# Kernel tuning notes

Hardware: AMD Instinct MI355X
Metric: run time of the kernel (lower is better)

The kernel has to match this reference:

```python
import jax, jax.numpy as jnp
import numpy as np

D_MODEL = 1024
N_HEADS = 16
HEAD_DIM = D_MODEL // N_HEADS


def setup_inputs() -> dict:
    key = jax.random.key(0)
    ks = jax.random.split(key, 5)
    B, S = 2, 2048
    x = jax.random.normal(ks[0], (B, S, D_MODEL), dtype=jnp.float32)
    # nn.Linear weights: [out_features, in_features]
    s_in = 1.0 / np.sqrt(D_MODEL)
    qkv_w = jax.random.uniform(ks[1], (3 * D_MODEL, D_MODEL), jnp.float32, -s_in, s_in)
    qkv_b = jax.random.uniform(ks[2], (3 * D_MODEL,), jnp.float32, -s_in, s_in)
    out_w = jax.random.uniform(ks[3], (D_MODEL, D_MODEL), jnp.float32, -s_in, s_in)
    out_b = jax.random.uniform(ks[4], (D_MODEL,), jnp.float32, -s_in, s_in)
    return {"x": x, "qkv_w": qkv_w, "qkv_b": qkv_b, "out_w": out_w, "out_b": out_b}


def reference(x, qkv_w, qkv_b, out_w, out_b):
    B, S, D = x.shape
    H, Hd = N_HEADS, HEAD_DIM
    scale = 1.0 / np.sqrt(Hd)
    qkv = jnp.einsum('bsd,ed->bse', x, qkv_w) + qkv_b  # [B,S,3D]
    qkv = qkv.reshape(B, S, 3, H, Hd)
    q = qkv[:, :, 0].transpose(0, 2, 1, 3)  # [B,H,S,Hd]
    k = qkv[:, :, 1].transpose(0, 2, 1, 3)
    v = qkv[:, :, 2].transpose(0, 2, 1, 3)
    scores = jnp.einsum('bhqd,bhkd->bhqk', q, k) * scale  # [B,H,S,S]
    causal = jnp.triu(jnp.ones((S, S), dtype=bool), k=1)
    scores = jnp.where(causal[None, None], -jnp.inf, scores)
    probs = jax.nn.softmax(scores, axis=-1)
    out = jnp.einsum('bhqk,bhkd->bhqd', probs, v)  # [B,H,S,Hd]
    out = out.transpose(0, 2, 1, 3).reshape(B, S, D)
    out = jnp.einsum('bsd,ed->bse', out, out_w) + out_b
    return out
```

## Files before the change

kernel.cpp:

```cpp
#include <hip/hip_runtime.h>
#include <hip/hip_bf16.h>

#define SEQ    2048
#define DMODEL 1024
#define NHEAD  16
#define HDIM   64
#define BATCH  2
#define NTOK   (BATCH * SEQ)

#define N_X   (NTOK * DMODEL)
#define N_WQ  (3 * DMODEL * DMODEL)
#define N_BQ  (3 * DMODEL)
#define N_WO  (DMODEL * DMODEL)
#define N_BO  (DMODEL)
#define N_CANON (N_X + N_WQ + N_BQ + N_WO + N_BO)

#define NEG_SENT (-1.0e30f)
#define QSCALE 0.1803368801111f

typedef __attribute__((ext_vector_type(8))) short short8;
typedef __attribute__((ext_vector_type(4))) short short4v;
typedef __attribute__((ext_vector_type(4))) float f32x4;

#define MFMA_BF16(A, B, C) __builtin_amdgcn_mfma_f32_16x16x32_bf16((A), (B), (C), 0, 0, 0)

static __device__ __forceinline__ short8 load8(const __hip_bfloat16* p) {
    return *(const short8*)p;
}

static __device__ __forceinline__ void async16(const void* g, void* l) {
    __builtin_amdgcn_global_load_lds(
        (const __attribute__((address_space(1))) unsigned int*)g,
        (__attribute__((address_space(3))) unsigned int*)l,
        16, 0, 0);
}

__global__ void detect_kernel(const unsigned short* __restrict__ w, int* flag) {
    int cnt = 0;
    for (int i = threadIdx.x; i < 512; i += 64) {
        const unsigned e = (w[i] >> 7) & 0xFF;
        if (e >= 125) cnt++;
    }
#pragma unroll
    for (int o = 32; o; o >>= 1) cnt += __shfl_down(cnt, o);
    if (threadIdx.x == 0) *flag = (cnt > 8) ? 1 : 0;
}

__global__ __launch_bounds__(256) void canon_kernel(
    const void* __restrict__ s0, const void* __restrict__ s1,
    const void* __restrict__ s2, const void* __restrict__ s3,
    const void* __restrict__ s4,
    __hip_bfloat16* __restrict__ dst, const int* __restrict__ flag)
{
    const int v = blockIdx.x * 256 + threadIdx.x;
    if (v >= N_CANON / 8) return;
    const int idx = v * 8;
    const void* src;
    int off;
    if (idx < N_X)                          { src = s0; off = idx; }
    else if (idx < N_X + N_WQ)              { src = s1; off = idx - N_X; }
    else if (idx < N_X + N_WQ + N_BQ)       { src = s2; off = idx - (N_X + N_WQ); }
    else if (idx < N_X + N_WQ + N_BQ + N_WO){ src = s3; off = idx - (N_X + N_WQ + N_BQ); }
    else                                    { src = s4; off = idx - (N_X + N_WQ + N_BQ + N_WO); }
    if (*flag != 0) {
        const f32x4* sp = (const f32x4*)((const float*)src + off);
        const f32x4 x0 = sp[0], x1 = sp[1];
        short8 o;
#pragma unroll
        for (int j = 0; j < 4; ++j) {
            o[j]     = (short)__bfloat16_as_ushort(__float2bfloat16(x0[j]));
            o[4 + j] = (short)__bfloat16_as_ushort(__float2bfloat16(x1[j]));
        }
        *(short8*)&dst[idx] = o;
    } else {
        *(short8*)&dst[idx] = *(const short8*)((const __hip_bfloat16*)src + off);
    }
}

__global__ __launch_bounds__(256) void qkv_gemm_kernel(
    const __hip_bfloat16* __restrict__ X,
    const __hip_bfloat16* __restrict__ W,
    const __hip_bfloat16* __restrict__ bias,
    __hip_bfloat16* __restrict__ Qs,
    __hip_bfloat16* __restrict__ Kb,
    __hip_bfloat16* __restrict__ Vt)
{
    constexpr int Kd = DMODEL;
    __shared__ __align__(16) __hip_bfloat16 As[2][128 * 32];
    __shared__ __align__(16) __hip_bfloat16 Bs[2][128 * 32];

    const int tid   = threadIdx.x;
    const int lane  = tid & 63;
    const int w     = tid >> 6;
    const int mTile = blockIdx.y * 128;
    const int nTile = blockIdx.x * 128;
    const int wm    = (w >> 1) * 64;
    const int wn    = (w & 1) * 64;
    const int lm    = lane & 15;
    const int q4    = lane >> 4;
    const int lks   = (q4 ^ ((lm >> 1) & 3)) * 8;

    f32x4 acc[4][4];
#pragma unroll
    for (int i = 0; i < 4; ++i)
#pragma unroll
        for (int j = 0; j < 4; ++j)
            acc[i][j] = (f32x4){0.f, 0.f, 0.f, 0.f};

    const int r0c = tid >> 2;
    const int r1c = (tid + 256) >> 2;
    const int cbs = ((tid & 3) ^ ((tid >> 3) & 3)) * 8;

    const __hip_bfloat16* gA0 = &X[(size_t)(mTile + r0c) * Kd + cbs];
    const __hip_bfloat16* gA1 = &X[(size_t)(mTile + r1c) * Kd + cbs];
    const __hip_bfloat16* gB0 = &W[(size_t)(nTile + r0c) * Kd + cbs];
    const __hip_bfloat16* gB1 = &W[(size_t)(nTile + r1c) * Kd + cbs];

    async16(gA0, (char*)As[0] + tid * 16);
    async16(gA1, (char*)As[0] + tid * 16 + 4096);
    async16(gB0, (char*)Bs[0] + tid * 16);
    async16(gB1, (char*)Bs[0] + tid * 16 + 4096);

    int cur = 0;
    constexpr int NIT = Kd / 32;
    for (int it = 0; it < NIT; ++it) {
        if (it + 1 < NIT) {
            const int k1 = (it + 1) * 32;
            async16(gA0 + k1, (char*)As[cur ^ 1] + tid * 16);
            async16(gA1 + k1, (char*)As[cur ^ 1] + tid * 16 + 4096);
            async16(gB0 + k1, (char*)Bs[cur ^ 1] + tid * 16);
            async16(gB1 + k1, (char*)Bs[cur ^ 1] + tid * 16 + 4096);
            asm volatile("s_waitcnt vmcnt(4)" ::: "memory");
        } else {
            asm volatile("s_waitcnt vmcnt(0)" ::: "memory");
        }
        __builtin_amdgcn_s_barrier();
        __builtin_amdgcn_sched_barrier(0);

        const __hip_bfloat16* Ac = As[cur];
        const __hip_bfloat16* Bc = Bs[cur];
        short8 a[4], b[4];
#pragma unroll
        for (int i = 0; i < 4; ++i)
            a[i] = *(const short8*)&Ac[(wm + i * 16 + lm) * 32 + lks];
#pragma unroll
        for (int j = 0; j < 4; ++j)
            b[j] = *(const short8*)&Bc[(wn + j * 16 + lm) * 32 + lks];
#pragma unroll
        for (int i = 0; i < 4; ++i)
#pragma unroll
            for (int j = 0; j < 4; ++j)
                acc[i][j] = MFMA_BF16(a[i], b[j], acc[i][j]);

        __builtin_amdgcn_s_barrier();
        cur ^= 1;
    }

    const int r0 = (lane >> 4) * 4;
#pragma unroll
    for (int j = 0; j < 4; ++j) {
        const int n  = nTile + wn + j * 16 + lm;
        const float bv = __bfloat162float(bias[n]);
        const int c = n >> 10;
        const int h = (n >> 6) & 15;
        const int d = n & 63;
#pragma unroll
        for (int i = 0; i < 4; ++i) {
            if (c == 2) {
                const int m0 = mTile + wm + i * 16 + r0;
                const int bb = m0 >> 11;
                const int s0 = m0 & (SEQ - 1);
                const int bh = bb * NHEAD + h;
                short4v pk;
#pragma unroll
                for (int r = 0; r < 4; ++r)
                    pk[r] = (short)__bfloat16_as_ushort(
                        __float2bfloat16(acc[i][j][r] + bv));
                *(short4v*)&Vt[(size_t)(bh * HDIM + d) * SEQ + s0] = pk;
            } else {
#pragma unroll
                for (int r = 0; r < 4; ++r) {
                    const int m  = mTile + wm + i * 16 + r0 + r;
                    const int bb = m >> 11;
                    const int s  = m & (SEQ - 1);
                    const int bh = bb * NHEAD + h;
                    const float v = acc[i][j][r] + bv;
                    if (c == 0) {
                        Qs[(size_t)(bh * SEQ + s) * HDIM + d] = __float2bfloat16(v * QSCALE);
                    } else {
                        Kb[(size_t)(bh * SEQ + s) * HDIM + d] = __float2bfloat16(v);
                    }
                }
            }
        }
    }
}

#define P_PITCH 72
__global__ __launch_bounds__(512, 4) void attn_kernel(
    const __hip_bfloat16* __restrict__ Qs,
    const __hip_bfloat16* __restrict__ Kb,
    const __hip_bfloat16* __restrict__ Vt,
    float* __restrict__ Opart,
    float* __restrict__ MLpart)
{
    __shared__ __align__(16) __hip_bfloat16 Kt[3][64 * 64];
    __shared__ __align__(16) __hip_bfloat16 Vs[3][64 * 64];
    __shared__ __align__(16) __hip_bfloat16 Pall[8][16 * P_PITCH];

    const int tid  = threadIdx.x;
    const int lane = tid & 63;
    const int wv   = tid >> 6;
    const int p    = blockIdx.x >> 1;
    const int kh   = blockIdx.x & 1;
    const int bh   = blockIdx.y;
    const int wgid = bh * 16 + blockIdx.x;

    const int lm  = lane & 15;
    const int q4  = lane >> 4;
    const int lk  = q4 * 8;
    const int swz = (lm & 3) << 4;

    __hip_bfloat16* P = Pall[wv];

    const __hip_bfloat16* Qbh = Qs + (size_t)bh * SEQ * HDIM;
    const __hip_bfloat16* Kbh = Kb + (size_t)bh * SEQ * HDIM;
    const __hip_bfloat16* Vbh = Vt + (size_t)bh * HDIM * SEQ;

    const int srow = tid >> 3;
    const int scb  = (tid & 7) ^ (srow & 7);

    for (int ph = 0; ph < 2; ++ph) {
        const int qb    = ph ? p : 15 - p;
        const int wbase = qb * 128 + wv * 16;
        const int nCh   = qb + 1;
        const int c0    = kh * nCh;

        short8 qa[2];
#pragma unroll
        for (int h = 0; h < 2; ++h)
            qa[h] = load8(&Qbh[(size_t)(wbase + lm) * HDIM + h * 32 + lk]);

        float m_run = NEG_SENT;
        float l_run = 0.f;
        f32x4 Oacc[4];
#pragma unroll
        for (int t = 0; t < 4; ++t) Oacc[t] = (f32x4){0.f, 0.f, 0.f, 0.f};

        __builtin_amdgcn_s_barrier();

        {
            const int kk0 = c0 * 64;
            async16(&Kbh[(size_t)(kk0 + srow) * HDIM + scb * 8], (char*)Kt[0] + tid * 16);
            async16(&Vbh[(size_t)srow * SEQ + kk0 + scb * 8],    (char*)Vs[0] + tid * 16);
            if (nCh >= 2) {
                const int kk1 = kk0 + 64;
                async16(&Kbh[(size_t)(kk1 + srow) * HDIM + scb * 8], (char*)Kt[1] + tid * 16);
                async16(&Vbh[(size_t)srow * SEQ + kk1 + scb * 8],    (char*)Vs[1] + tid * 16);
            }
        }

        int cur = 0;
        for (int ci = 0; ci < nCh; ++ci) {
            const int k0 = (c0 + ci) * 64;

            if (ci + 1 < nCh) {
                asm volatile("s_waitcnt vmcnt(2)" ::: "memory");
            } else {
                asm volatile("s_waitcnt vmcnt(0)" ::: "memory");
            }
            __builtin_amdgcn_s_barrier();
            __builtin_amdgcn_sched_barrier(0);

            if (ci + 2 < nCh) {
                const int slot = (cur + 2 >= 3) ? cur - 1 : cur + 2;
                const int kk = (c0 + ci + 2) * 64;
                async16(&Kbh[(size_t)(kk + srow) * HDIM + scb * 8], (char*)Kt[slot] + tid * 16);
                async16(&Vbh[(size_t)srow * SEQ + kk + scb * 8],    (char*)Vs[slot] + tid * 16);
            }

            if (k0 <= wbase + 15) {
                const __hip_bfloat16* Kc = Kt[cur];
                const __hip_bfloat16* Vc = Vs[cur];

                short8 ka[4][2];
#pragma unroll
                for (int t = 0; t < 4; ++t)
#pragma unroll
                    for (int h = 0; h < 2; ++h)
                        ka[t][h] = *(const short8*)&Kc[(t * 16 + lm) * 64 +
                                                       (((h * 4 + q4) ^ (lm & 7)) * 8)];

                f32x4 sc[4];
#pragma unroll
                for (int t = 0; t < 4; ++t) sc[t] = (f32x4){0.f, 0.f, 0.f, 0.f};
                __builtin_amdgcn_s_setprio(1);
#pragma unroll
                for (int t = 0; t < 4; ++t) {
                    sc[t] = MFMA_BF16(ka[t][0], qa[0], sc[t]);
                    sc[t] = MFMA_BF16(ka[t][1], qa[1], sc[t]);
                }
                __builtin_amdgcn_s_setprio(0);

                if (k0 + 63 > wbase) {
                    const int row = wbase + lm;
#pragma unroll
                    for (int t = 0; t < 4; ++t)
#pragma unroll
                        for (int r = 0; r < 4; ++r) {
                            const int key = k0 + t * 16 + q4 * 4 + r;
                            if (key > row) sc[t][r] = NEG_SENT;
                        }
                }

                float mx = sc[0][0];
#pragma unroll
                for (int t = 0; t < 4; ++t)
#pragma unroll
                    for (int r = 0; r < 4; ++r) mx = fmaxf(mx, sc[t][r]);
                mx = fmaxf(mx, __shfl_xor(mx, 16));
                mx = fmaxf(mx, __shfl_xor(mx, 32));

                if (!__all(mx <= m_run + 8.0f)) {
                    const float mn = fmaxf(m_run, mx);
                    const float alpha = exp2f(m_run - mn);
                    m_run = mn;
                    l_run *= alpha;
#pragma unroll
                    for (int r = 0; r < 4; ++r) {
                        const float av = __shfl(alpha, q4 * 4 + r);
#pragma unroll
                        for (int t = 0; t < 4; ++t) Oacc[t][r] *= av;
                    }
                }

                float s = 0.f;
#pragma unroll
                for (int t = 0; t < 4; ++t)
#pragma unroll
                    for (int r = 0; r < 4; ++r) {
                        const float pv = exp2f(sc[t][r] - m_run);
                        sc[t][r] = pv;
                        s += pv;
                    }
                s += __shfl_xor(s, 16);
                s += __shfl_xor(s, 32);
                l_run += s;

#pragma unroll
                for (int t = 0; t < 4; ++t) {
                    short4v pk;
#pragma unroll
                    for (int r = 0; r < 4; ++r)
                        pk[r] = (short)__bfloat16_as_ushort(__float2bfloat16(sc[t][r]));
                    const int col = (t * 16 + q4 * 4) ^ swz;
                    *(short4v*)&P[lm * P_PITCH + col] = pk;
                }

                __builtin_amdgcn_s_setprio(1);
#pragma unroll
                for (int h = 0; h < 2; ++h) {
                    const short8 pa = *(const short8*)&P[lm * P_PITCH + ((h * 32 + lk) ^ swz)];
#pragma unroll
                    for (int t = 0; t < 4; ++t) {
                        const short8 vb = *(const short8*)&Vc[(t * 16 + lm) * 64 +
                                                              (((h * 4 + q4) ^ (lm & 7)) * 8)];
                        Oacc[t] = MFMA_BF16(pa, vb, Oacc[t]);
                    }
                }
                __builtin_amdgcn_s_setprio(0);
            }

            cur = (cur + 1 == 3) ? 0 : cur + 1;
        }

        const size_t pbase = ((size_t)wgid * 2 + ph) * 128;
#pragma unroll
        for (int t = 0; t < 4; ++t)
#pragma unroll
            for (int r = 0; r < 4; ++r)
                Opart[(pbase + wv * 16 + q4 * 4 + r) * 64 + t * 16 + lm] = Oacc[t][r];
        if (lane < 16) {
            MLpart[(pbase + wv * 16 + lane) * 2 + 0] = m_run;
            MLpart[(pbase + wv * 16 + lane) * 2 + 1] = l_run;
        }
    }
}

__global__ __launch_bounds__(256) void attn_merge_kernel(
    const float* __restrict__ Opart, const float* __restrict__ MLpart,
    __hip_bfloat16* __restrict__ O)
{
    const int idx  = blockIdx.x * 256 + threadIdx.x;
    const int d16  = idx & 3;
    const int grow = idx >> 2;
    const int bh   = grow >> 11;
    const int s    = grow & 2047;
    const int qb   = s >> 7;
    const int rin  = s & 127;
    const int p    = (qb >= 8) ? (15 - qb) : qb;
    const int ph   = (qb >= 8) ? 0 : 1;
    const size_t r0 = ((size_t)(bh * 16 + p * 2 + 0) * 2 + ph) * 128 + rin;
    const size_t r1 = ((size_t)(bh * 16 + p * 2 + 1) * 2 + ph) * 128 + rin;

    const float m1 = MLpart[r0 * 2], l1 = MLpart[r0 * 2 + 1];
    const float m2 = MLpart[r1 * 2], l2 = MLpart[r1 * 2 + 1];
    const float mm = fmaxf(m1, m2);
    const float a1 = exp2f(m1 - mm), a2 = exp2f(m2 - mm);
    const float inv = 1.0f / (a1 * l1 + a2 * l2);

    const f32x4* O1 = (const f32x4*)&Opart[r0 * 64 + d16 * 16];
    const f32x4* O2 = (const f32x4*)&Opart[r1 * 64 + d16 * 16];

    short8 out[2];
#pragma unroll
    for (int v = 0; v < 4; ++v) {
        const f32x4 x1 = O1[v], x2 = O2[v];
#pragma unroll
        for (int j = 0; j < 4; ++j)
            out[v >> 1][(v & 1) * 4 + j] = (short)__bfloat16_as_ushort(
                __float2bfloat16((a1 * x1[j] + a2 * x2[j]) * inv));
    }
    const int b = bh >> 4, hh = bh & 15;
    __hip_bfloat16* dst = &O[((size_t)b * SEQ + s) * DMODEL + hh * 64 + d16 * 16];
    ((short8*)dst)[0] = out[0];
    ((short8*)dst)[1] = out[1];
}

__global__ __launch_bounds__(256) void proj_gemm_kernel(
    const __hip_bfloat16* __restrict__ A,
    const __hip_bfloat16* __restrict__ W,
    const __hip_bfloat16* __restrict__ bias,
    void* __restrict__ outv,
    const int* __restrict__ flag)
{
    constexpr int Kd = DMODEL;
    __shared__ __align__(16) __hip_bfloat16 As[2][128 * 32];
    __shared__ __align__(16) __hip_bfloat16 Bs[2][64 * 32];

    const int tid   = threadIdx.x;
    const int lane  = tid & 63;
    const int w     = tid >> 6;
    const int mTile = blockIdx.y * 128;
    const int nTile = blockIdx.x * 64;
    const int wm    = (w >> 1) * 64;
    const int wn    = (w & 1) * 32;
    const int lm    = lane & 15;
    const int q4    = lane >> 4;
    const int lks   = (q4 ^ ((lm >> 1) & 3)) * 8;
    const bool f32out = (*flag != 0);

    f32x4 acc[4][2];
#pragma unroll
    for (int i = 0; i < 4; ++i)
#pragma unroll
        for (int j = 0; j < 2; ++j)
            acc[i][j] = (f32x4){0.f, 0.f, 0.f, 0.f};

    const int r0c = tid >> 2;
    const int r1c = (tid + 256) >> 2;
    const int cbs = ((tid & 3) ^ ((tid >> 3) & 3)) * 8;

    const __hip_bfloat16* gA0 = &A[(size_t)(mTile + r0c) * Kd + cbs];
    const __hip_bfloat16* gA1 = &A[(size_t)(mTile + r1c) * Kd + cbs];
    const __hip_bfloat16* gB0 = &W[(size_t)(nTile + r0c) * Kd + cbs];

    async16(gA0, (char*)As[0] + tid * 16);
    async16(gA1, (char*)As[0] + tid * 16 + 4096);
    async16(gB0, (char*)Bs[0] + tid * 16);

    int cur = 0;
    constexpr int NIT = Kd / 32;
    for (int it = 0; it < NIT; ++it) {
        if (it + 1 < NIT) {
            const int k1 = (it + 1) * 32;
            async16(gA0 + k1, (char*)As[cur ^ 1] + tid * 16);
            async16(gA1 + k1, (char*)As[cur ^ 1] + tid * 16 + 4096);
            async16(gB0 + k1, (char*)Bs[cur ^ 1] + tid * 16);
            asm volatile("s_waitcnt vmcnt(3)" ::: "memory");
        } else {
            asm volatile("s_waitcnt vmcnt(0)" ::: "memory");
        }
        __builtin_amdgcn_s_barrier();
        __builtin_amdgcn_sched_barrier(0);

        const __hip_bfloat16* Ac = As[cur];
        const __hip_bfloat16* Bc = Bs[cur];
        short8 a[4], b[2];
#pragma unroll
        for (int i = 0; i < 4; ++i)
            a[i] = *(const short8*)&Ac[(wm + i * 16 + lm) * 32 + lks];
#pragma unroll
        for (int j = 0; j < 2; ++j)
            b[j] = *(const short8*)&Bc[(wn + j * 16 + lm) * 32 + lks];
#pragma unroll
        for (int i = 0; i < 4; ++i)
#pragma unroll
            for (int j = 0; j < 2; ++j)
                acc[i][j] = MFMA_BF16(a[i], b[j], acc[i][j]);

        __builtin_amdgcn_s_barrier();
        cur ^= 1;
    }

    const int r0 = (lane >> 4) * 4;
#pragma unroll
    for (int j = 0; j < 2; ++j) {
        const int n = nTile + wn + j * 16 + lm;
        const float bv = __bfloat162float(bias[n]);
#pragma unroll
        for (int i = 0; i < 4; ++i) {
#pragma unroll
            for (int r = 0; r < 4; ++r) {
                const size_t m = mTile + wm + i * 16 + r0 + r;
                const float v = acc[i][j][r] + bv;
                if (f32out) ((float*)outv)[m * DMODEL + n] = v;
                else ((__hip_bfloat16*)outv)[m * DMODEL + n] = __float2bfloat16(v);
            }
        }
    }
}

extern "C" void kernel_launch(void* const* d_in, const int* in_sizes, int n_in,
                              void* d_out, int out_size, void* d_ws, size_t ws_size,
                              hipStream_t stream) {
    const size_t OFF_CANON = 256;
    const size_t OFF_QS = OFF_CANON + (size_t)N_CANON * 2;
    const size_t OFF_KB = OFF_QS + (size_t)NTOK * DMODEL * 2;
    const size_t OFF_VT = OFF_KB + (size_t)NTOK * DMODEL * 2;
    const size_t OFF_AO = OFF_VT + (size_t)NTOK * DMODEL * 2;
    const size_t OFF_OP = OFF_AO + (size_t)NTOK * DMODEL * 2;
    const size_t OFF_ML = OFF_OP + (size_t)512 * 2 * 128 * 64 * 4;

    char* wsb = (char*)d_ws;
    int* flag = (int*)wsb;
    __hip_bfloat16* canon = (__hip_bfloat16*)(wsb + OFF_CANON);
    __hip_bfloat16* Xc = canon;
    __hip_bfloat16* Wq = Xc + N_X;
    __hip_bfloat16* Bq = Wq + N_WQ;
    __hip_bfloat16* Wo = Bq + N_BQ;
    __hip_bfloat16* Bo = Wo + N_WO;
    __hip_bfloat16* Qs = (__hip_bfloat16*)(wsb + OFF_QS);
    __hip_bfloat16* Kb = (__hip_bfloat16*)(wsb + OFF_KB);
    __hip_bfloat16* Vt = (__hip_bfloat16*)(wsb + OFF_VT);
    __hip_bfloat16* Ao = (__hip_bfloat16*)(wsb + OFF_AO);
    float* Opart = (float*)(wsb + OFF_OP);
    float* MLpart = (float*)(wsb + OFF_ML);

    detect_kernel<<<1, 64, 0, stream>>>((const unsigned short*)d_in[1], flag);
    canon_kernel<<<(N_CANON / 8 + 255) / 256, 256, 0, stream>>>(
        d_in[0], d_in[1], d_in[2], d_in[3], d_in[4], canon, flag);

    {
        dim3 grid(3 * DMODEL / 128, NTOK / 128);
        qkv_gemm_kernel<<<grid, 256, 0, stream>>>(Xc, Wq, Bq, Qs, Kb, Vt);
    }
    {
        dim3 grid(16, BATCH * NHEAD);
        attn_kernel<<<grid, 512, 0, stream>>>(Qs, Kb, Vt, Opart, MLpart);
        attn_merge_kernel<<<(NTOK * NHEAD * 4) / 256, 256, 0, stream>>>(
            Opart, MLpart, Ao);
    }
    {
        dim3 grid(DMODEL / 64, NTOK / 128);
        proj_gemm_kernel<<<grid, 256, 0, stream>>>(Ao, Wo, Bo, d_out, flag);
    }
}
```

Before: 192.2 us.

## Split causal attention work into three balanced chunk ranges per query-block pair

The attention grid moves from 16x32 blocks, each splitting a query-block pair's keys in half, to 32x24 blocks. Each block takes one of three balanced contiguous ranges of key chunks over the combined heavy-plus-light pair, and the merge kernel combines up to three partials. The K/V ring drops from three buffers to two with an extra barrier before each prefetch, and launch bounds rise to allow more resident blocks. This aims to balance load and raise occupancy, at the cost of more partial writes, more merge reads and less prefetch depth.

```diff
diff --git a/kernel.cpp b/kernel.cpp
--- a/kernel.cpp
+++ b/kernel.cpp
@@ -197,24 +197,28 @@
 }
 
 #define P_PITCH 72
-__global__ __launch_bounds__(512, 4) void attn_kernel(
+__global__ __launch_bounds__(512, 6) void attn_kernel(
     const __hip_bfloat16* __restrict__ Qs,
     const __hip_bfloat16* __restrict__ Kb,
     const __hip_bfloat16* __restrict__ Vt,
     float* __restrict__ Opart,
     float* __restrict__ MLpart)
 {
-    __shared__ __align__(16) __hip_bfloat16 Kt[3][64 * 64];
-    __shared__ __align__(16) __hip_bfloat16 Vs[3][64 * 64];
+    __shared__ __align__(16) __hip_bfloat16 Kt[2][64 * 64];
+    __shared__ __align__(16) __hip_bfloat16 Vs[2][64 * 64];
     __shared__ __align__(16) __hip_bfloat16 Pall[8][16 * P_PITCH];
 
     const int tid  = threadIdx.x;
     const int lane = tid & 63;
     const int wv   = tid >> 6;
-    const int p    = blockIdx.x >> 1;
-    const int kh   = blockIdx.x & 1;
-    const int bh   = blockIdx.y;
-    const int wgid = bh * 16 + blockIdx.x;
+    const int bh   = blockIdx.x;
+    const int py   = blockIdx.y;
+    const int p    = py / 3;
+    const int j3   = py % 3;
+
+    const int c_lo = (j3 == 0) ? 0 : (j3 == 1 ? 12 : 23);
+    const int c_hi = (j3 == 0) ? 12 : (j3 == 1 ? 23 : 34);
+    const int bnd  = 32 - 2 * p;
 
     const int lm  = lane & 15;
     const int q4  = lane >> 4;
@@ -230,11 +234,22 @@
     const int srow = tid >> 3;
     const int scb  = (tid & 7) ^ (srow & 7);
 
-    for (int ph = 0; ph < 2; ++ph) {
-        const int qb    = ph ? p : 15 - p;
+    for (int seg = 0; seg < 2; ++seg) {
+        int qb, a, b, slot;
+        if (seg == 0) {
+            if (j3 == 2 && p >= 5) continue;
+            qb = 15 - p; a = c_lo;
+            b  = (c_hi < bnd) ? c_hi : bnd;
+            slot = j3;
+        } else {
+            if (j3 == 0 || (j3 == 1 && p <= 4)) continue;
+            qb = p;
+            a  = ((c_lo > bnd) ? c_lo : bnd) - bnd;
+            b  = c_hi - bnd;
+            slot = (j3 == 2) ? 3 : 4;
+        }
+
         const int wbase = qb * 128 + wv * 16;
-        const int nCh   = qb + 1;
-        const int c0    = kh * nCh;
 
         short8 qa[2];
 #pragma unroll
@@ -250,10 +265,10 @@
         __builtin_amdgcn_s_barrier();
 
         {
-            const int kk0 = c0 * 64;
+            const int kk0 = a * 64;
             async16(&Kbh[(size_t)(kk0 + srow) * HDIM + scb * 8], (char*)Kt[0] + tid * 16);
             async16(&Vbh[(size_t)srow * SEQ + kk0 + scb * 8],    (char*)Vs[0] + tid * 16);
-            if (nCh >= 2) {
+            if (a + 1 < b) {
                 const int kk1 = kk0 + 64;
                 async16(&Kbh[(size_t)(kk1 + srow) * HDIM + scb * 8], (char*)Kt[1] + tid * 16);
                 async16(&Vbh[(size_t)srow * SEQ + kk1 + scb * 8],    (char*)Vs[1] + tid * 16);
@@ -261,10 +276,10 @@
         }
 
         int cur = 0;
-        for (int ci = 0; ci < nCh; ++ci) {
-            const int k0 = (c0 + ci) * 64;
-
-            if (ci + 1 < nCh) {
+        for (int ci = a; ci < b; ++ci) {
+            const int k0 = ci * 64;
+
+            if (ci + 1 < b) {
                 asm volatile("s_waitcnt vmcnt(2)" ::: "memory");
             } else {
                 asm volatile("s_waitcnt vmcnt(0)" ::: "memory");
@@ -272,13 +287,6 @@
             __builtin_amdgcn_s_barrier();
             __builtin_amdgcn_sched_barrier(0);
 
-            if (ci + 2 < nCh) {
-                const int slot = (cur + 2 >= 3) ? cur - 1 : cur + 2;
-                const int kk = (c0 + ci + 2) * 64;
-                async16(&Kbh[(size_t)(kk + srow) * HDIM + scb * 8], (char*)Kt[slot] + tid * 16);
-                async16(&Vbh[(size_t)srow * SEQ + kk + scb * 8],    (char*)Vs[slot] + tid * 16);
-            }
-
             if (k0 <= wbase + 15) {
                 const __hip_bfloat16* Kc = Kt[cur];
                 const __hip_bfloat16* Vc = Vs[cur];
@@ -294,13 +302,11 @@
                 f32x4 sc[4];
 #pragma unroll
                 for (int t = 0; t < 4; ++t) sc[t] = (f32x4){0.f, 0.f, 0.f, 0.f};
-                __builtin_amdgcn_s_setprio(1);
 #pragma unroll
                 for (int t = 0; t < 4; ++t) {
                     sc[t] = MFMA_BF16(ka[t][0], qa[0], sc[t]);
                     sc[t] = MFMA_BF16(ka[t][1], qa[1], sc[t]);
                 }
-                __builtin_amdgcn_s_setprio(0);
 
                 if (k0 + 63 > wbase) {
                     const int row = wbase + lm;
@@ -357,7 +363,6 @@
                     *(short4v*)&P[lm * P_PITCH + col] = pk;
                 }
 
-                __builtin_amdgcn_s_setprio(1);
 #pragma unroll
                 for (int h = 0; h < 2; ++h) {
                     const short8 pa = *(const short8*)&P[lm * P_PITCH + ((h * 32 + lk) ^ swz)];
@@ -368,13 +373,18 @@
                         Oacc[t] = MFMA_BF16(pa, vb, Oacc[t]);
                     }
                 }
-                __builtin_amdgcn_s_setprio(0);
             }
 
-            cur = (cur + 1 == 3) ? 0 : cur + 1;
-        }
-
-        const size_t pbase = ((size_t)wgid * 2 + ph) * 128;
+            __builtin_amdgcn_s_barrier();
+            if (ci + 2 < b) {
+                const int kk = (ci + 2) * 64;
+                async16(&Kbh[(size_t)(kk + srow) * HDIM + scb * 8], (char*)Kt[cur] + tid * 16);
+                async16(&Vbh[(size_t)srow * SEQ + kk + scb * 8],    (char*)Vs[cur] + tid * 16);
+            }
+            cur ^= 1;
+        }
+
+        const size_t pbase = ((size_t)(bh * 8 + p) * 5 + slot) * 128;
 #pragma unroll
         for (int t = 0; t < 4; ++t)
 #pragma unroll
@@ -398,29 +408,54 @@
     const int s    = grow & 2047;
     const int qb   = s >> 7;
     const int rin  = s & 127;
-    const int p    = (qb >= 8) ? (15 - qb) : qb;
-    const int ph   = (qb >= 8) ? 0 : 1;
-    const size_t r0 = ((size_t)(bh * 16 + p * 2 + 0) * 2 + ph) * 128 + rin;
-    const size_t r1 = ((size_t)(bh * 16 + p * 2 + 1) * 2 + ph) * 128 + rin;
-
-    const float m1 = MLpart[r0 * 2], l1 = MLpart[r0 * 2 + 1];
-    const float m2 = MLpart[r1 * 2], l2 = MLpart[r1 * 2 + 1];
-    const float mm = fmaxf(m1, m2);
-    const float a1 = exp2f(m1 - mm), a2 = exp2f(m2 - mm);
-    const float inv = 1.0f / (a1 * l1 + a2 * l2);
-
-    const f32x4* O1 = (const f32x4*)&Opart[r0 * 64 + d16 * 16];
-    const f32x4* O2 = (const f32x4*)&Opart[r1 * 64 + d16 * 16];
+
+    const bool heavy = (qb >= 8);
+    const int p  = heavy ? (15 - qb) : qb;
+    const int s0 = heavy ? 0 : 3;
+    const int s1 = heavy ? 1 : 4;
+    const bool v1 = heavy ? true : (p >= 5);
+    const bool v2 = heavy && (p <= 4);
+
+    const size_t rb = (size_t)(bh * 8 + p) * 5;
+    const size_t r0 = (rb + s0) * 128 + rin;
+    const size_t r1 = (rb + s1) * 128 + rin;
+    const size_t r2 = (rb + 2)  * 128 + rin;
+
+    const float m0 = MLpart[r0 * 2],                 l0 = MLpart[r0 * 2 + 1];
+    const float m1 = v1 ? MLpart[r1 * 2] : NEG_SENT, l1 = v1 ? MLpart[r1 * 2 + 1] : 0.f;
+    const float m2 = v2 ? MLpart[r2 * 2] : NEG_SENT, l2 = v2 ? MLpart[r2 * 2 + 1] : 0.f;
+
+    float mm = fmaxf(m0, fmaxf(m1, m2));
+    const float a0 = exp2f(m0 - mm);
+    const float a1 = v1 ? exp2f(m1 - mm) : 0.f;
+    const float a2 = v2 ? exp2f(m2 - mm) : 0.f;
+    const float inv = 1.0f / (a0 * l0 + a1 * l1 + a2 * l2);
+
+    f32x4 o[4];
+    {
+        const f32x4* O0 = (const f32x4*)&Opart[r0 * 64 + d16 * 16];
+#pragma unroll
+        for (int v = 0; v < 4; ++v) o[v] = a0 * O0[v];
+    }
+    if (v1) {
+        const f32x4* O1 = (const f32x4*)&Opart[r1 * 64 + d16 * 16];
+#pragma unroll
+        for (int v = 0; v < 4; ++v) o[v] += a1 * O1[v];
+    }
+    if (v2) {
+        const f32x4* O2 = (const f32x4*)&Opart[r2 * 64 + d16 * 16];
+#pragma unroll
+        for (int v = 0; v < 4; ++v) o[v] += a2 * O2[v];
+    }
 
     short8 out[2];
 #pragma unroll
-    for (int v = 0; v < 4; ++v) {
-        const f32x4 x1 = O1[v], x2 = O2[v];
-#pragma unroll
-        for (int j = 0; j < 4; ++j)
-            out[v >> 1][(v & 1) * 4 + j] = (short)__bfloat16_as_ushort(
-                __float2bfloat16((a1 * x1[j] + a2 * x2[j]) * inv));
-    }
+    for (int v = 0; v < 4; ++v)
+#pragma unroll
+        for (int jj = 0; jj < 4; ++jj)
+            out[v >> 1][(v & 1) * 4 + jj] = (short)__bfloat16_as_ushort(
+                __float2bfloat16(o[v][jj] * inv));
+
     const int b = bh >> 4, hh = bh & 15;
     __hip_bfloat16* dst = &O[((size_t)b * SEQ + s) * DMODEL + hh * 64 + d16 * 16];
     ((short8*)dst)[0] = out[0];
@@ -530,7 +565,7 @@
     const size_t OFF_VT = OFF_KB + (size_t)NTOK * DMODEL * 2;
     const size_t OFF_AO = OFF_VT + (size_t)NTOK * DMODEL * 2;
     const size_t OFF_OP = OFF_AO + (size_t)NTOK * DMODEL * 2;
-    const size_t OFF_ML = OFF_OP + (size_t)512 * 2 * 128 * 64 * 4;
+    const size_t OFF_ML = OFF_OP + (size_t)32 * 8 * 5 * 128 * 64 * 4;
 
     char* wsb = (char*)d_ws;
     int* flag = (int*)wsb;
@@ -556,7 +591,7 @@
         qkv_gemm_kernel<<<grid, 256, 0, stream>>>(Xc, Wq, Bq, Qs, Kb, Vt);
     }
     {
-        dim3 grid(16, BATCH * NHEAD);
+        dim3 grid(BATCH * NHEAD, 24);
         attn_kernel<<<grid, 512, 0, stream>>>(Qs, Kb, Vt, Opart, MLpart);
         attn_merge_kernel<<<(NTOK * NHEAD * 4) / 256, 256, 0, stream>>>(
             Opart, MLpart, Ao);
```

After: 190.6 us. No clear change (-0.8%).
